# Kernel optimization log

Measured on AMD Instinct MI355X. Metric: run time of the kernel, lower is better.

The kernel has to match this reference:

```python
import jax, jax.numpy as jnp
import numpy as np
from jax import lax

B, T, I, H = 64, 512, 256, 256


def setup_inputs() -> dict:
    key = jax.random.key(0)
    ks = jax.random.split(key, 5)
    s_in = 1.0 / np.sqrt(I)
    s_h = 1.0 / np.sqrt(H)
    return {
        "x": jax.random.normal(ks[0], (B, T, I), dtype=jnp.float32),
        "W0": jax.random.normal(ks[1], (I, 4 * H), dtype=jnp.float32) * s_in,
        "U0": jax.random.normal(ks[2], (H, 4 * H), dtype=jnp.float32) * s_h,
        "b0": jnp.zeros((4 * H,), dtype=jnp.float32),
        "W1": jax.random.normal(ks[3], (H, 4 * H), dtype=jnp.float32) * s_h,
        "U1": jax.random.normal(ks[4], (H, 4 * H), dtype=jnp.float32) * s_h,
        "b1": jnp.zeros((4 * H,), dtype=jnp.float32),
    }


def _lstm_layer(x, W, U, b):
    # x: [B, T, Din]; W: [Din, 4H]; U: [H, 4H]; b: [4H]
    h_dim = U.shape[0]
    batch = x.shape[0]
    # Precompute input projections for all timesteps in one GEMM.
    xz = jnp.einsum('bti,ig->btg', x, W) + b  # [B, T, 4H]

    def step(carry, xzt):
        h, c = carry
        z = xzt + h @ U  # [B, 4H]
        i, f, g, o = jnp.split(z, 4, axis=-1)
        c = jax.nn.sigmoid(f) * c + jax.nn.sigmoid(i) * jnp.tanh(g)
        h = jax.nn.sigmoid(o) * jnp.tanh(c)
        return (h, c), h

    init = (jnp.zeros((batch, h_dim), x.dtype), jnp.zeros((batch, h_dim), x.dtype))
    _, hs = lax.scan(step, init, jnp.swapaxes(xz, 0, 1))  # hs: [T, B, H]
    return jnp.swapaxes(hs, 0, 1)  # [B, T, H]


def reference(x, W0, U0, b0, W1, U1, b1):
    y = _lstm_layer(x, W0, U0, b0)
    y = _lstm_layer(y, W1, U1, b1)
    return y
```

## Files before the change

### kernel.cpp

```cpp
#include <hip/hip_runtime.h>

typedef unsigned short ushort_t;
typedef unsigned int uint_t;

using f16x8 = __attribute__((ext_vector_type(8))) _Float16;
using f32x4 = __attribute__((ext_vector_type(4))) float;
using u32x4 = __attribute__((ext_vector_type(4))) unsigned int;

#define BATCH 64
#define SEQT 512
#define DIN 256
#define HID 256
#define G4 1024
#define CH 16
#define NCH (SEQT / CH)

static __device__ __forceinline__ ushort_t f16b(float x) {
    return __builtin_bit_cast(ushort_t, (_Float16)x);
}
static __device__ __forceinline__ float f16f(ushort_t u) {
    return (float)__builtin_bit_cast(_Float16, u);
}
static __device__ __forceinline__ uint_t pk2(float a, float b) {
    return (uint_t)f16b(a) | ((uint_t)f16b(b) << 16);
}
static __device__ __forceinline__ float sig_(float x) {
    return 1.f / (1.f + __expf(-x));
}
static __device__ __forceinline__ float tanh_(float x) {
    float e = __expf(2.f * x);
    return (e - 1.f) / (e + 1.f);
}

#define PINA(x) asm volatile("" : "+a"(x))
#define PINV(x) asm volatile("" : "+v"(x))

static __device__ __forceinline__ f16x8 asf16(u32x4 v) {
    return __builtin_bit_cast(f16x8, v);
}


__global__ void prep_all_kernel(
    const float* __restrict__ x,
    const float* __restrict__ W0, const float* __restrict__ W1,
    const float* __restrict__ U0, const float* __restrict__ U1,
    ushort_t* __restrict__ xf16,
    ushort_t* __restrict__ Wt0, ushort_t* __restrict__ Wt1,
    uint4* __restrict__ Upk0, uint4* __restrict__ Upk1)
{
    int blk = blockIdx.x;
    int tid = threadIdx.x;
    if (blk < 8192) {
        int i = blk * 256 + tid;
        float4 v = ((const float4*)x)[i];
        ushort4 o;
        o.x = f16b(v.x); o.y = f16b(v.y); o.z = f16b(v.z); o.w = f16b(v.w);
        ((ushort4*)xf16)[i] = o;
    } else if (blk < 10240) {
        const float* W = (blk < 9216) ? W0 : W1;
        ushort_t* Wt = (blk < 9216) ? Wt0 : Wt1;
        int t = ((blk - 8192) & 1023) * 256 + tid;
        int k = t >> 10;
        int n = t & 1023;
        Wt[n * DIN + k] = f16b(W[t]);
    } else {
        const float* U = (blk < 10368) ? U0 : U1;
        uint4* Upk = (blk < 10368) ? Upk0 : Upk1;
        int t = ((blk - 10240) & 127) * 256 + tid;
        int j = t >> 10;
        int g = t & 1023;
        uint4 o;
        uint_t* op = &o.x;
#pragma unroll
        for (int q = 0; q < 4; ++q) {
            float a = U[(8 * j + 2 * q) * G4 + g];
            float bb = U[(8 * j + 2 * q + 1) * G4 + g];
            op[q] = pk2(a, bb);
        }
        Upk[t] = o;
    }
}


#define GSTRIDE 40

__global__ __launch_bounds__(256) void gemm_f16_kernel(
    const ushort_t* __restrict__ A,
    const ushort_t* __restrict__ Bt,
    const float* __restrict__ bias,
    ushort_t* __restrict__ C,
    int M)
{
    const int K = DIN, N = G4;
    __shared__ ushort_t As[128 * GSTRIDE];
    __shared__ ushort_t Bs[128 * GSTRIDE];
    int tid = threadIdx.x;
    int bx = blockIdx.x & 7;
    int by = blockIdx.x >> 3;
    int m0 = by * 128, n0 = bx * 128;
    int w = tid >> 6, lane = tid & 63;
    int wr = (w >> 1) * 64, wc = (w & 1) * 64;
    int r = lane & 15, kg = lane >> 4;

    f32x4 acc[4][4];
#pragma unroll
    for (int i = 0; i < 4; ++i)
#pragma unroll
        for (int j = 0; j < 4; ++j)
            acc[i][j] = f32x4{0.f, 0.f, 0.f, 0.f};

    for (int kt = 0; kt < K; kt += 32) {
        __syncthreads();
#pragma unroll
        for (int s = 0; s < 2; ++s) {
            int chunk = tid + s * 256;
            int row = chunk >> 2;
            int ko = (chunk & 3) * 8;
            uint4 va = *(const uint4*)(A + (size_t)(m0 + row) * K + kt + ko);
            *(uint4*)(&As[row * GSTRIDE + ko]) = va;
            uint4 vb = *(const uint4*)(Bt + (size_t)(n0 + row) * K + kt + ko);
            *(uint4*)(&Bs[row * GSTRIDE + ko]) = vb;
        }
        __syncthreads();
        f16x8 af[4], bf[4];
#pragma unroll
        for (int i = 0; i < 4; ++i) {
            af[i] = *(const f16x8*)(&As[(wr + i * 16 + r) * GSTRIDE + kg * 8]);
            bf[i] = *(const f16x8*)(&Bs[(wc + i * 16 + r) * GSTRIDE + kg * 8]);
        }
#pragma unroll
        for (int i = 0; i < 4; ++i)
#pragma unroll
            for (int j = 0; j < 4; ++j)
                acc[i][j] = __builtin_amdgcn_mfma_f32_16x16x32_f16(af[i], bf[j], acc[i][j], 0, 0, 0);
    }

#pragma unroll
    for (int i = 0; i < 4; ++i)
#pragma unroll
        for (int j = 0; j < 4; ++j) {
            int col = n0 + wc + j * 16 + r;
            float bv = bias[col];
#pragma unroll
            for (int v = 0; v < 4; ++v) {
                int rowg = m0 + wr + i * 16 + kg * 4 + v;
                C[(size_t)rowg * N + col] = f16b(acc[i][j][v] + bv);
            }
        }
}


__global__ __launch_bounds__(256)
__attribute__((amdgpu_waves_per_eu(1, 1)))
void lstm_pipe3_kernel(
    const ushort_t* __restrict__ xz1h,
    const u32x4* __restrict__ Upk0,
    const u32x4* __restrict__ Upk1,
    const ushort_t* __restrict__ Wt1,
    const float* __restrict__ b1,
    uint_t* y1pk,
    int* flag1, int* flag2, int* flag3,
    uint_t* xz2u,
    float* __restrict__ out,
    int T)
{
    __shared__ __align__(16) u32x4 Uld[4][2][16][64];
    __shared__ __align__(16) ushort_t ys[32][264];
    __shared__ __align__(16) ushort_t h16[2][HID];

    const int tid = threadIdx.x;
    const int w = tid >> 6;
    const int l = tid & 63;
    const int lg = l >> 4;
    const int lr = l & 15;
    const int role = (int)(blockIdx.x >> 6);
    const int b = (int)(blockIdx.x & 63);
    const int hcol = w * 64 + lg * 16 + lr;

    int* f1p = flag1 + b * 32;
    int* f2p = flag2 + b * 32;
    int* f3p = flag3 + b * 32;

    if (role == 1) {
        float b1w[16];
#pragma unroll
        for (int ct = 0; ct < 16; ++ct) b1w[ct] = b1[(w * 16 + ct) * 16 + lr];
        __syncthreads();

        for (int ch = 0; ch < NCH; ++ch) {
            if (tid == 0) {
                while (__hip_atomic_load(f1p, __ATOMIC_ACQUIRE, __HIP_MEMORY_SCOPE_AGENT) < ch + 1)
                    __builtin_amdgcn_s_sleep(32);
                while (__hip_atomic_load(f3p, __ATOMIC_ACQUIRE, __HIP_MEMORY_SCOPE_AGENT) < ch - 3)
                    __builtin_amdgcn_s_sleep(32);
            }
            __syncthreads();

#pragma unroll
            for (int it = 0; it < 8; ++it) {
                int idx = it * 256 + tid;
                int row = idx >> 7;
                int j = idx & 127;
                uint_t v = __hip_atomic_load(
                    &y1pk[(size_t)(b * T + ch * CH + row) * 128 + j],
                    __ATOMIC_RELAXED, __HIP_MEMORY_SCOPE_AGENT);
                *(uint_t*)&ys[row][2 * j] = v;
            }
            __syncthreads();

            uint_t* xzbuf = xz2u + ((size_t)(b * 4 + (ch & 3)) * CH) * G4;
#pragma unroll
            for (int ct = 0; ct < 16; ++ct) {
                int ctI = w * 16 + ct;
                u32x4 bf[8];
#pragma unroll
                for (int kt = 0; kt < 8; ++kt)
                    bf[kt] = *(const u32x4*)(Wt1 + (size_t)(ctI * 16 + lr) * DIN + kt * 32 + lg * 8);
                f32x4 acc = f32x4{0.f, 0.f, 0.f, 0.f};
#pragma unroll
                for (int kt = 0; kt < 8; ++kt) {
                    f16x8 af = *(const f16x8*)&ys[lr][kt * 32 + lg * 8];
                    acc = __builtin_amdgcn_mfma_f32_16x16x32_f16(af, asf16(bf[kt]), acc, 0, 0, 0);
                }
#pragma unroll
                for (int v = 0; v < 4; ++v) {
                    float z = acc[v] + b1w[ct];
                    __hip_atomic_store(&xzbuf[(size_t)(lg * 4 + v) * G4 + ctI * 16 + lr],
                                       __builtin_bit_cast(uint_t, z),
                                       __ATOMIC_RELAXED, __HIP_MEMORY_SCOPE_AGENT);
                }
            }
            __syncthreads();
            if (tid == 0)
                __hip_atomic_store(f2p, ch + 1, __ATOMIC_RELEASE, __HIP_MEMORY_SCOPE_AGENT);
        }
        return;
    }

    const u32x4* Upk = (role == 2) ? Upk1 : Upk0;
    u32x4 ua[64];
    u32x4 uv[32];
#pragma unroll
    for (int gb = 0; gb < 4; ++gb)
#pragma unroll
        for (int ti = 0; ti < 4; ++ti) {
            int col = (gb * 16 + w * 4 + ti) * 16 + lr;
            int fi = gb * 4 + ti;
#pragma unroll
            for (int kt = 0; kt < 4; ++kt)
                ua[fi * 4 + kt] = Upk[(kt * 4 + lg) * 1024 + col];
#pragma unroll
            for (int k2 = 0; k2 < 2; ++k2)
                uv[fi * 2 + k2] = Upk[((4 + k2) * 4 + lg) * 1024 + col];
        }
#pragma unroll
    for (int i = 0; i < 64; ++i) PINA(ua[i]);
#pragma unroll
    for (int i = 0; i < 32; ++i) PINV(uv[i]);

#pragma unroll
    for (int gb = 0; gb < 4; ++gb)
#pragma unroll
        for (int ti = 0; ti < 4; ++ti) {
            int col = (gb * 16 + w * 4 + ti) * 16 + lr;
            int fi = gb * 4 + ti;
#pragma unroll
            for (int k2 = 0; k2 < 2; ++k2)
                Uld[w][k2][fi][l] = Upk[((6 + k2) * 4 + lg) * 1024 + col];
        }

    h16[0][tid] = 0;
    float c = 0.f;

#define STEP_BODY(AF, XZC, ZG)                                                        \
    {                                                                                 \
        _Pragma("unroll")                                                             \
        for (int gb = 0; gb < 4; ++gb) {                                              \
            f32x4 accA[4], accB[4];                                                   \
            _Pragma("unroll")                                                         \
            for (int ti = 0; ti < 4; ++ti) {                                          \
                accA[ti] = f32x4{0.f, 0.f, 0.f, 0.f};                                 \
                accB[ti] = f32x4{0.f, 0.f, 0.f, 0.f};                                 \
            }                                                                         \
            _Pragma("unroll")                                                         \
            for (int ti = 0; ti < 4; ++ti) {                                          \
                int fi = gb * 4 + ti;                                                 \
                _Pragma("unroll")                                                     \
                for (int kt = 0; kt < 4; ++kt)                                        \
                    accA[ti] = __builtin_amdgcn_mfma_f32_16x16x32_f16(                \
                        AF[kt], asf16(ua[fi * 4 + kt]), accA[ti], 0, 0, 0);           \
                _Pragma("unroll")                                                     \
                for (int k2 = 0; k2 < 2; ++k2)                                        \
                    accB[ti] = __builtin_amdgcn_mfma_f32_16x16x32_f16(                \
                        AF[4 + k2], asf16(uv[fi * 2 + k2]), accB[ti], 0, 0, 0);       \
                _Pragma("unroll")                                                     \
                for (int k2 = 0; k2 < 2; ++k2) {                                      \
                    u32x4 ub = Uld[w][k2][fi][l];                                     \
                    accB[ti] = __builtin_amdgcn_mfma_f32_16x16x32_f16(                \
                        AF[6 + k2], asf16(ub), accB[ti], 0, 0, 0);                    \
                }                                                                     \
            }                                                                         \
            float za = (lg == 0) ? accA[0][0] : (lg == 1) ? accA[1][0]                \
                     : (lg == 2) ? accA[2][0] : accA[3][0];                           \
            float zb = (lg == 0) ? accB[0][0] : (lg == 1) ? accB[1][0]                \
                     : (lg == 2) ? accB[2][0] : accB[3][0];                           \
            ZG[gb] = za + zb + XZC[gb];                                               \
        }                                                                             \
    }

    if (role == 0) {
        uint_t* hr = (uint_t*)&ys[0][0];
        const ushort_t* xz_b = xz1h + (size_t)b * T * G4;
        float xzc[4];
#pragma unroll
        for (int gb = 0; gb < 4; ++gb) xzc[gb] = f16f(xz_b[gb * 256 + hcol]);
        __syncthreads();

        for (int t = 0; t < T; ++t) {
            const int cur = t & 1, nxt = cur ^ 1;

            f16x8 af[8];
#pragma unroll
            for (int kt = 0; kt < 8; ++kt)
                af[kt] = *(const f16x8*)((const char*)&h16[cur][0] + kt * 64 + lg * 16);

            float xzn[4];
            {
                const ushort_t* xztn = xz_b + (size_t)((t + 1 < T) ? (t + 1) : t) * G4;
#pragma unroll
                for (int gb = 0; gb < 4; ++gb) xzn[gb] = f16f(xztn[gb * 256 + hcol]);
            }

            float zg[4];
            STEP_BODY(af, xzc, zg);

            c = sig_(zg[1]) * c + sig_(zg[0]) * tanh_(zg[2]);
            float h = sig_(zg[3]) * tanh_(c);

            h16[nxt][hcol] = f16b(h);
            {
                uint_t hb = (uint_t)f16b(h);
                uint_t pb = (uint_t)(unsigned)__shfl_xor((int)hb, 1);
                if (!(l & 1))
                    hr[(t & (CH - 1)) * 128 + (hcol >> 1)] = hb | (pb << 16);
            }
#pragma unroll
            for (int gb = 0; gb < 4; ++gb) xzc[gb] = xzn[gb];

            __syncthreads();

            if ((t & (CH - 1)) == (CH - 1)) {
                int t0 = t - (CH - 1);
#pragma unroll
                for (int it = 0; it < 8; ++it) {
                    int idx = it * 256 + tid;
                    int row = idx >> 7;
                    int j = idx & 127;
                    __hip_atomic_store(&y1pk[(size_t)(b * T + t0 + row) * 128 + j],
                                       hr[row * 128 + j],
                                       __ATOMIC_RELAXED, __HIP_MEMORY_SCOPE_AGENT);
                }
                __syncthreads();
                if (tid == 0)
                    __hip_atomic_store(f1p, (t + 1) / CH, __ATOMIC_RELEASE,
                                       __HIP_MEMORY_SCOPE_AGENT);
            }
        }
    } else {
        float* orb = (float*)&ys[0][0];
        __syncthreads();

        for (int ch = 0; ch < NCH; ++ch) {
            if (tid == 0) {
                while (__hip_atomic_load(f2p, __ATOMIC_ACQUIRE, __HIP_MEMORY_SCOPE_AGENT) < ch + 1)
                    __builtin_amdgcn_s_sleep(32);
            }
            __syncthreads();

            const uint_t* xzbuf = xz2u + ((size_t)(b * 4 + (ch & 3)) * CH) * G4;
            uint_t xzw[4], xznw[4];

            for (int tb = 0; tb < CH; ++tb) {
                const int t = ch * CH + tb;
                const int cur = t & 1, nxt = cur ^ 1;

                if (tb == 0) {
#pragma unroll
                    for (int gb = 0; gb < 4; ++gb)
                        xzw[gb] = __hip_atomic_load(&xzbuf[gb * 256 + hcol],
                                                    __ATOMIC_RELAXED, __HIP_MEMORY_SCOPE_AGENT);
                } else {
#pragma unroll
                    for (int gb = 0; gb < 4; ++gb) xzw[gb] = xznw[gb];
                }

                f16x8 af[8];
#pragma unroll
                for (int kt = 0; kt < 8; ++kt)
                    af[kt] = *(const f16x8*)((const char*)&h16[cur][0] + kt * 64 + lg * 16);

                if (tb + 1 < CH) {
#pragma unroll
                    for (int gb = 0; gb < 4; ++gb)
                        xznw[gb] = __hip_atomic_load(
                            &xzbuf[(size_t)(tb + 1) * G4 + gb * 256 + hcol],
                            __ATOMIC_RELAXED, __HIP_MEMORY_SCOPE_AGENT);
                }

                float xzc[4];
#pragma unroll
                for (int gb = 0; gb < 4; ++gb)
                    xzc[gb] = __builtin_bit_cast(float, xzw[gb]);

                float zg[4];
                STEP_BODY(af, xzc, zg);

                c = sig_(zg[1]) * c + sig_(zg[0]) * tanh_(zg[2]);
                float h = sig_(zg[3]) * tanh_(c);

                h16[nxt][hcol] = f16b(h);
                orb[tb * 256 + hcol] = h;

                __syncthreads();
            }

#pragma unroll
            for (int it = 0; it < 16; ++it) {
                int idx = it * 256 + tid;
                int row = idx >> 8;
                int col = idx & 255;
                out[(size_t)(b * T + ch * CH + row) * HID + col] = orb[row * 256 + col];
            }
            if (tid == 0)
                __hip_atomic_store(f3p, ch + 1, __ATOMIC_RELEASE, __HIP_MEMORY_SCOPE_AGENT);
        }
    }
#undef STEP_BODY
}


extern "C" void kernel_launch(void* const* d_in, const int* in_sizes, int n_in,
                              void* d_out, int out_size, void* d_ws, size_t ws_size,
                              hipStream_t stream) {
    const float* x  = (const float*)d_in[0];
    const float* W0 = (const float*)d_in[1];
    const float* U0 = (const float*)d_in[2];
    const float* b0 = (const float*)d_in[3];
    const float* W1 = (const float*)d_in[4];
    const float* U1 = (const float*)d_in[5];
    const float* b1 = (const float*)d_in[6];
    float* out = (float*)d_out;

    const size_t M = (size_t)BATCH * SEQT;

    char* ws = (char*)d_ws;
    ushort_t* xf16  = (ushort_t*)(ws);
    uint_t*   y1pk  = (uint_t*)  (ws + (16u << 20));
    ushort_t* Wt0   = (ushort_t*)(ws + (32u << 20));
    ushort_t* Wt1   = (ushort_t*)(ws + (32u << 20) + 524288);
    u32x4*    Upk0  = (u32x4*)   (ws + (33u << 20));
    u32x4*    Upk1  = (u32x4*)   (ws + (33u << 20) + 524288);
    int*      flag1 = (int*)     (ws + (34u << 20));
    int*      flag2 = (int*)     (ws + (34u << 20) + 65536);
    int*      flag3 = (int*)     (ws + (34u << 20) + 131072);
    uint_t*   xz2u  = (uint_t*)  (ws + (35u << 20));
    ushort_t* xz1h  = (ushort_t*)(ws + (51u << 20));

    hipMemsetAsync(flag1, 0, 196608, stream);

    prep_all_kernel<<<dim3(10496), dim3(256), 0, stream>>>(
        x, W0, W1, U0, U1, xf16, Wt0, Wt1, (uint4*)Upk0, (uint4*)Upk1);

    gemm_f16_kernel<<<dim3((int)(M / 128) * 8), dim3(256), 0, stream>>>(xf16, Wt0, b0, xz1h, (int)M);

    lstm_pipe3_kernel<<<dim3(192), dim3(256), 0, stream>>>(
        xz1h, Upk0, Upk1, Wt1, b1, y1pk, flag1, flag2, flag3, xz2u, out, SEQT);
}
```

Before: 1.120 ms.

## Split recurrent MFMA into early/late phases so one barrier per step suffices

Each wave first computes the MFMA k-slices of h that it produced itself (its own h columns) before a barrier, then the remaining k-slices after it. This lets the per-step end-of-step barrier be removed, leaving one barrier per timestep, and moves the h fragment loads into the phases. The intent is to shorten the serial critical path of the recurrence. The correctness of the double-buffered h16 depends on the wave-to-k mapping matching who writes which h columns, and the changed reduction order alters accumulation rounding.

```diff
diff --git a/kernel.cpp b/kernel.cpp
--- a/kernel.cpp
+++ b/kernel.cpp
@@ -272,41 +272,33 @@
     h16[0][tid] = 0;
     float c = 0.f;
 
-#define STEP_BODY(AF, XZC, ZG)                                                        \
-    {                                                                                 \
-        _Pragma("unroll")                                                             \
-        for (int gb = 0; gb < 4; ++gb) {                                              \
-            f32x4 accA[4], accB[4];                                                   \
-            _Pragma("unroll")                                                         \
-            for (int ti = 0; ti < 4; ++ti) {                                          \
-                accA[ti] = f32x4{0.f, 0.f, 0.f, 0.f};                                 \
-                accB[ti] = f32x4{0.f, 0.f, 0.f, 0.f};                                 \
-            }                                                                         \
-            _Pragma("unroll")                                                         \
-            for (int ti = 0; ti < 4; ++ti) {                                          \
-                int fi = gb * 4 + ti;                                                 \
-                _Pragma("unroll")                                                     \
-                for (int kt = 0; kt < 4; ++kt)                                        \
-                    accA[ti] = __builtin_amdgcn_mfma_f32_16x16x32_f16(                \
-                        AF[kt], asf16(ua[fi * 4 + kt]), accA[ti], 0, 0, 0);           \
-                _Pragma("unroll")                                                     \
-                for (int k2 = 0; k2 < 2; ++k2)                                        \
-                    accB[ti] = __builtin_amdgcn_mfma_f32_16x16x32_f16(                \
-                        AF[4 + k2], asf16(uv[fi * 2 + k2]), accB[ti], 0, 0, 0);       \
-                _Pragma("unroll")                                                     \
-                for (int k2 = 0; k2 < 2; ++k2) {                                      \
-                    u32x4 ub = Uld[w][k2][fi][l];                                     \
-                    accB[ti] = __builtin_amdgcn_mfma_f32_16x16x32_f16(                \
-                        AF[6 + k2], asf16(ub), accB[ti], 0, 0, 0);                    \
-                }                                                                     \
-            }                                                                         \
-            float za = (lg == 0) ? accA[0][0] : (lg == 1) ? accA[1][0]                \
-                     : (lg == 2) ? accA[2][0] : accA[3][0];                           \
-            float zb = (lg == 0) ? accB[0][0] : (lg == 1) ? accB[1][0]                \
-                     : (lg == 2) ? accB[2][0] : accB[3][0];                           \
-            ZG[gb] = za + zb + XZC[gb];                                               \
-        }                                                                             \
-    }
+#define AFRD(KT) (*(const f16x8*)((const char*)&h16[cur][0] + (KT) * 64 + lg * 16))
+#define FRAG(KT, FI) ((KT) < 4 ? ua[(FI) * 4 + (KT)] \
+                    : (KT) < 6 ? uv[(FI) * 2 + ((KT) - 4)] \
+                    : Uld[w][(KT) - 6][FI][l])
+
+#define PHASE_EARLY(KA, KB) {                                                          \
+        f16x8 af0 = AFRD(KA), af1 = AFRD(KB);                                          \
+        _Pragma("unroll") for (int gb = 0; gb < 4; ++gb)                               \
+        _Pragma("unroll") for (int ti = 0; ti < 4; ++ti) {                             \
+            int fi = gb * 4 + ti;                                                      \
+            f32x4 z0 = f32x4{0.f, 0.f, 0.f, 0.f};                                      \
+            z0 = __builtin_amdgcn_mfma_f32_16x16x32_f16(af0, asf16(FRAG(KA, fi)), z0, 0, 0, 0); \
+            acc[gb][ti] = __builtin_amdgcn_mfma_f32_16x16x32_f16(af1, asf16(FRAG(KB, fi)), z0, 0, 0, 0); \
+        } }
+
+#define PHASE_LATE(KA, KB) {                                                           \
+        _Pragma("unroll") for (int kt = 0; kt < 8; ++kt) {                             \
+            if (kt == (KA) || kt == (KB)) continue;                                    \
+            f16x8 afk = AFRD(kt);                                                      \
+            _Pragma("unroll") for (int gb = 0; gb < 4; ++gb)                           \
+            _Pragma("unroll") for (int ti = 0; ti < 4; ++ti) {                         \
+                int fi = gb * 4 + ti;                                                  \
+                acc[gb][ti] = __builtin_amdgcn_mfma_f32_16x16x32_f16(afk, asf16(FRAG(kt, fi)), acc[gb][ti], 0, 0, 0); \
+            } } }
+
+#define ACCSEL(GB) ((lg == 0) ? acc[GB][0][0] : (lg == 1) ? acc[GB][1][0] \
+                  : (lg == 2) ? acc[GB][2][0] : acc[GB][3][0])
 
     if (role == 0) {
         uint_t* hr = (uint_t*)&ys[0][0];
@@ -319,11 +311,6 @@
         for (int t = 0; t < T; ++t) {
             const int cur = t & 1, nxt = cur ^ 1;
 
-            f16x8 af[8];
-#pragma unroll
-            for (int kt = 0; kt < 8; ++kt)
-                af[kt] = *(const f16x8*)((const char*)&h16[cur][0] + kt * 64 + lg * 16);
-
             float xzn[4];
             {
                 const ushort_t* xztn = xz_b + (size_t)((t + 1 < T) ? (t + 1) : t) * G4;
@@ -331,8 +318,20 @@
                 for (int gb = 0; gb < 4; ++gb) xzn[gb] = f16f(xztn[gb * 256 + hcol]);
             }
 
+            f32x4 acc[4][4];
+            if (w == 0)      PHASE_EARLY(0, 1)
+            else if (w == 1) PHASE_EARLY(2, 3)
+            else if (w == 2) PHASE_EARLY(4, 5)
+            else             PHASE_EARLY(6, 7)
+            __syncthreads();
+            if (w == 0)      PHASE_LATE(0, 1)
+            else if (w == 1) PHASE_LATE(2, 3)
+            else if (w == 2) PHASE_LATE(4, 5)
+            else             PHASE_LATE(6, 7)
+
             float zg[4];
-            STEP_BODY(af, xzc, zg);
+#pragma unroll
+            for (int gb = 0; gb < 4; ++gb) zg[gb] = ACCSEL(gb) + xzc[gb];
 
             c = sig_(zg[1]) * c + sig_(zg[0]) * tanh_(zg[2]);
             float h = sig_(zg[3]) * tanh_(c);
@@ -347,9 +346,8 @@
 #pragma unroll
             for (int gb = 0; gb < 4; ++gb) xzc[gb] = xzn[gb];
 
-            __syncthreads();
-
             if ((t & (CH - 1)) == (CH - 1)) {
+                __syncthreads();
                 int t0 = t - (CH - 1);
 #pragma unroll
                 for (int it = 0; it < 8; ++it) {
@@ -394,11 +392,6 @@
                     for (int gb = 0; gb < 4; ++gb) xzw[gb] = xznw[gb];
                 }
 
-                f16x8 af[8];
-#pragma unroll
-                for (int kt = 0; kt < 8; ++kt)
-                    af[kt] = *(const f16x8*)((const char*)&h16[cur][0] + kt * 64 + lg * 16);
-
                 if (tb + 1 < CH) {
 #pragma unroll
                     for (int gb = 0; gb < 4; ++gb)
@@ -407,13 +400,21 @@
                             __ATOMIC_RELAXED, __HIP_MEMORY_SCOPE_AGENT);
                 }
 
-                float xzc[4];
+                f32x4 acc[4][4];
+                if (w == 0)      PHASE_EARLY(0, 1)
+                else if (w == 1) PHASE_EARLY(2, 3)
+                else if (w == 2) PHASE_EARLY(4, 5)
+                else             PHASE_EARLY(6, 7)
+                __syncthreads();
+                if (w == 0)      PHASE_LATE(0, 1)
+                else if (w == 1) PHASE_LATE(2, 3)
+                else if (w == 2) PHASE_LATE(4, 5)
+                else             PHASE_LATE(6, 7)
+
+                float zg[4];
 #pragma unroll
                 for (int gb = 0; gb < 4; ++gb)
-                    xzc[gb] = __builtin_bit_cast(float, xzw[gb]);
-
-                float zg[4];
-                STEP_BODY(af, xzc, zg);
+                    zg[gb] = ACCSEL(gb) + __builtin_bit_cast(float, xzw[gb]);
 
                 c = sig_(zg[1]) * c + sig_(zg[0]) * tanh_(zg[2]);
                 float h = sig_(zg[3]) * tanh_(c);
@@ -421,21 +422,26 @@
                 h16[nxt][hcol] = f16b(h);
                 orb[tb * 256 + hcol] = h;
 
-                __syncthreads();
-            }
-
-#pragma unroll
-            for (int it = 0; it < 16; ++it) {
-                int idx = it * 256 + tid;
-                int row = idx >> 8;
-                int col = idx & 255;
-                out[(size_t)(b * T + ch * CH + row) * HID + col] = orb[row * 256 + col];
-            }
-            if (tid == 0)
-                __hip_atomic_store(f3p, ch + 1, __ATOMIC_RELEASE, __HIP_MEMORY_SCOPE_AGENT);
+                if (tb == CH - 1) {
+                    __syncthreads();
+#pragma unroll
+                    for (int it = 0; it < 16; ++it) {
+                        int idx = it * 256 + tid;
+                        int row = idx >> 8;
+                        int col = idx & 255;
+                        out[(size_t)(b * T + ch * CH + row) * HID + col] = orb[row * 256 + col];
+                    }
+                    if (tid == 0)
+                        __hip_atomic_store(f3p, ch + 1, __ATOMIC_RELEASE, __HIP_MEMORY_SCOPE_AGENT);
+                }
+            }
         }
     }
-#undef STEP_BODY
+#undef PHASE_EARLY
+#undef PHASE_LATE
+#undef AFRD
+#undef FRAG
+#undef ACCSEL
 }
 
 
```

Result: slower. 3.764 ms (+235.9%).
